# Performance work log

Hardware: AMD Instinct MI355X
Metric: run time of the kernel (lower is better)

The kernel has to match this reference:

```python
import jax, jax.numpy as jnp
import numpy as np

B, I, H, MS, M = 8192, 1024, 1024, 64, 16
TAU = 1.0


def setup_inputs() -> dict:
    key = jax.random.key(0)
    ks = jax.random.split(key, 24)
    s = 0.02
    eps = 1e-6
    return {
        "x": jax.random.normal(ks[0], (B, I), jnp.float32),
        "h": jax.random.normal(ks[1], (B, H), jnp.float32),
        "c": jax.random.normal(ks[2], (B, H), jnp.float32),
        "memory": jax.random.normal(ks[3], (B, M, MS), jnp.float32),
        "u_gs": jax.random.uniform(ks[4], (B, M), jnp.float32, eps, 1.0 - eps),
        "u_a": jax.random.uniform(ks[5], (B, 1), jnp.float32, eps, 1.0 - eps),
        "u_b": jax.random.uniform(ks[6], (B, 1), jnp.float32, eps, 1.0 - eps),
        # pre-concatenated gate weights, matching torch.cat((W_x2*, W_h2*, W_c2*), 0)
        "W_i": jax.random.normal(ks[7], (I + 2 * H, H), jnp.float32) * s,
        "b_i": jnp.zeros((H,), jnp.float32),
        "W_f": jax.random.normal(ks[8], (I + 2 * H, H), jnp.float32) * s,
        "b_f": jnp.ones((H,), jnp.float32),
        "W_o": jax.random.normal(ks[9], (I + 2 * H, H), jnp.float32) * s,
        "b_o": jnp.zeros((H,), jnp.float32),
        "W_cand": jax.random.normal(ks[10], (I + H, H), jnp.float32) * s,
        "b_cand": jnp.zeros((H,), jnp.float32),
        "W_m": jax.random.normal(ks[11], (H, MS), jnp.float32) * s,
        "b_m": jnp.zeros((MS,), jnp.float32),
        "w_a_h": jax.random.normal(ks[12], (H, 1), jnp.float32) * s,
        "w_a_x": jax.random.normal(ks[13], (I, 1), jnp.float32) * s,
        "w_a_r": jax.random.normal(ks[14], (MS, 1), jnp.float32) * s,
        "w_b_h": jax.random.normal(ks[15], (H, 1), jnp.float32) * s,
        "w_b_x": jax.random.normal(ks[16], (I, 1), jnp.float32) * s,
        "w_b_r": jax.random.normal(ks[17], (MS, 1), jnp.float32) * s,
    }


def reference(x, h, c, memory, u_gs, u_a, u_b,
              W_i, b_i, W_f, b_f, W_o, b_o, W_cand, b_cand,
              W_m, b_m, w_a_h, w_a_x, w_a_r, w_b_h, w_b_x, w_b_r):
    # LSTM-style gates with peephole c in the concatenated input
    xhc = jnp.concatenate([x, h, c], axis=1)            # [B, I+2H]
    i = jax.nn.sigmoid(xhc @ W_i + b_i)
    f = jax.nn.sigmoid(xhc @ W_f + b_f)
    cp = jnp.tanh(jnp.concatenate([x, h], axis=1) @ W_cand + b_cand)
    c_new = f * c + i * cp
    o = jax.nn.sigmoid(jnp.concatenate([x, h, c_new], axis=1) @ W_o + b_o)
    h_new = o * jnp.tanh(c_new)

    # memory-slot attention with Gumbel-softmax sampling
    micro = h_new @ W_m + b_m                           # [B, MS]
    logits = jnp.einsum('bmk,bk->bm', memory, micro)    # [B, M]
    g = -jnp.log(-jnp.log(u_gs))                        # Gumbel(0,1)
    attn = jax.nn.softmax((logits + g) / TAU, axis=-1)  # sampled_locations
    sampled = jnp.einsum('bmk,bm->bk', memory, attn) + 1.0  # [B, MS]

    # gumbel-sigmoid (binary concrete) for alpha / beta
    la = jnp.log(u_a) - jnp.log1p(-u_a)
    lb = jnp.log(u_b) - jnp.log1p(-u_b)
    alpha = jax.nn.sigmoid((h_new @ w_a_h + x @ w_a_x + sampled @ w_a_r + la) / TAU)
    beta = jax.nn.sigmoid((h_new @ w_b_h + x @ w_b_x + sampled @ w_b_r + lb) / TAU)

    # [B, 2H+2]
    return jnp.concatenate([h_new, c_new, alpha, beta], axis=1)
```

## Files before the change

### kernel.cpp

```cpp
#include <hip/hip_runtime.h>

typedef __bf16 bfrag __attribute__((ext_vector_type(8)));
typedef float f32x4 __attribute__((ext_vector_type(4)));

#define GLDS16(g, l) __builtin_amdgcn_global_load_lds( \
    (__attribute__((address_space(1))) void*)(g),      \
    (__attribute__((address_space(3))) void*)(l), 16, 0, 0)

__device__ __forceinline__ float bf2f(ushort u) {
    return __uint_as_float(((unsigned)u) << 16);
}
__device__ __forceinline__ ushort f2bf(float f) {
    unsigned u = __float_as_uint(f);
    u += 0x7fff + ((u >> 16) & 1);
    return (ushort)(u >> 16);
}
__device__ __forceinline__ float sigmoidf_(float v) {
    return 1.0f / (1.0f + expf(-v));
}

struct TD { const float* src; ushort* dst; int src_ld; int dst_ld; int ktiles; int off; };
struct TA { TD d[6]; };

__global__ __launch_bounds__(256) void k_prep(const float* __restrict__ x,
                                              const float* __restrict__ h,
                                              const float* __restrict__ c,
                                              ushort* __restrict__ xhcb, TA a,
                                              const float* __restrict__ bi,
                                              const float* __restrict__ bf_,
                                              const float* __restrict__ bc,
                                              const float* __restrict__ bo,
                                              float* __restrict__ Biasf) {
    __shared__ float tile[64][65];
    int bid = blockIdx.x;
    int t = threadIdx.x;
    if (bid < 12288) {
        int idx = bid * 256 + t;
        int row = idx / 384;
        int c8 = (idx - row * 384) * 8;
        const float* s = (c8 < 1024) ? &x[(size_t)row * 1024 + c8]
                       : (c8 < 2048) ? &h[(size_t)row * 1024 + (c8 - 1024)]
                                     : &c[(size_t)row * 1024 + (c8 - 2048)];
        float4 va = *(const float4*)s;
        float4 vb = *(const float4*)(s + 4);
        ushort tmp[8] = {f2bf(va.x), f2bf(va.y), f2bf(va.z), f2bf(va.w),
                         f2bf(vb.x), f2bf(vb.y), f2bf(vb.z), f2bf(vb.w)};
        *(uint4*)&xhcb[(size_t)idx * 8] = *(uint4*)tmp;
    } else if (bid < 15120) {
        int tb = bid - 12288;
        int ri = 0;
#pragma unroll
        for (int i = 1; i < 6; ++i) ri = (tb >= a.d[i].off) ? i : ri;
        const float* src = a.d[ri].src;
        ushort* dst = a.d[ri].dst;
        int src_ld = a.d[ri].src_ld, dst_ld = a.d[ri].dst_ld;
        int local = tb - a.d[ri].off;
        int bx = local % a.d[ri].ktiles;
        int by = local / a.d[ri].ktiles;
        int k0 = bx * 64, n0 = by * 64;
        int c4 = (t & 15) * 4;
        int r = t >> 4;
#pragma unroll
        for (int i = 0; i < 4; ++i) {
            int rr = r + i * 16;
            float4 v = *(const float4*)&src[(size_t)(k0 + rr) * src_ld + n0 + c4];
            tile[rr][c4 + 0] = v.x; tile[rr][c4 + 1] = v.y;
            tile[rr][c4 + 2] = v.z; tile[rr][c4 + 3] = v.w;
        }
        __syncthreads();
        int kk8 = (t & 7) * 8;
        int nn = t >> 3;
#pragma unroll
        for (int i = 0; i < 2; ++i) {
            int n = nn + i * 32;
            ushort tmp[8];
#pragma unroll
            for (int j = 0; j < 8; ++j) tmp[j] = f2bf(tile[kk8 + j][n]);
            *(uint4*)&dst[(size_t)(n0 + n) * dst_ld + k0 + kk8] = *(uint4*)tmp;
        }
    } else {
        int idx = (bid - 15120) * 256 + t;
        int g = idx >> 10, n = idx & 1023;
        const float* s = (g == 0) ? bi : (g == 1) ? bf_ : (g == 2) ? bc : bo;
        Biasf[idx] = s[n];
    }
}

__global__ __launch_bounds__(512) void k_gemm1(const ushort* __restrict__ xhcb,
                                               const ushort* __restrict__ WT,
                                               const float* __restrict__ bias,
                                               ushort* __restrict__ Pre) {
    __shared__ __align__(16) ushort lds[2][32768];
    const int t = threadIdx.x;
    const int m0 = blockIdx.x * 256;
    const int by = blockIdx.y;
    const int n0 = by * 256;
    const int KTOT = (by < 8) ? 3072 : 2048;
    const int NT = KTOT >> 6;
    const int w = t >> 6, l = t & 63;
    const int wr = w >> 2, wc = w & 3;
    const int lane16 = l & 15, quad = l >> 4;
    const int r7 = lane16 & 7;
    const int rowt = t >> 3;
    const int kg = (t & 7) ^ (rowt & 7);
    const int brow_hi = rowt >> 5, brow_lo = rowt & 31;
    f32x4 acc[8][4] = {};
    bfrag afr[4][2];
    bfrag bfr[2][2][2];

    const ushort* Ag = xhcb + (size_t)(m0 + rowt) * 3072 + kg * 8;
    const ushort* Bg = WT + (size_t)(n0 + brow_lo) * 3072 + kg * 8;

#define STAGE_A(BUF, PI, KT)                                                       \
    do {                                                                           \
        GLDS16(Ag + (size_t)((PI) * 64) * 3072 + (KT) * 64,                        \
               &lds[BUF][((PI) * 64) * 64] + t * 8);                               \
        GLDS16(Ag + (size_t)((PI) * 64 + 128) * 3072 + (KT) * 64,                  \
               &lds[BUF][((PI) * 64 + 128) * 64] + t * 8);                         \
    } while (0)

#define STAGE_B(BUF, PI, KT)                                                       \
    do {                                                                           \
        GLDS16(Bg + (size_t)((PI) * 32 + brow_hi * 64) * 3072 + (KT) * 64,         \
               &lds[BUF][16384 + ((PI) * 128) * 64] + t * 8);                      \
        GLDS16(Bg + (size_t)((PI) * 32 + (2 + brow_hi) * 64) * 3072 + (KT) * 64,   \
               &lds[BUF][16384 + ((PI) * 128 + 64) * 64] + t * 8);                 \
    } while (0)

#define LDA(QM)                                                                           \
    do {                                                                                  \
        _Pragma("unroll") for (int ii = 0; ii < 4; ++ii) {                                \
            _Pragma("unroll") for (int h = 0; h < 2; ++h)                                 \
                afr[ii][h] = *(const bfrag*)&Acur[(wr * 128 + (QM) * 64 + ii * 16 + lane16) * 64 + \
                                                  (((h * 4 + quad) ^ r7) * 8)];           \
        }                                                                                 \
    } while (0)

#define LDB(QN)                                                                           \
    do {                                                                                  \
        _Pragma("unroll") for (int jj = 0; jj < 2; ++jj) {                                \
            _Pragma("unroll") for (int h = 0; h < 2; ++h)                                 \
                bfr[QN][jj][h] = *(const bfrag*)&Bcur[((QN) * 128 + wc * 32 + jj * 16 + lane16) * 64 + \
                                                      (((h * 4 + quad) ^ r7) * 8)];       \
        }                                                                                 \
    } while (0)

#define MM(QM, QN)                                                                        \
    do {                                                                                  \
        __builtin_amdgcn_s_setprio(1);                                                    \
        _Pragma("unroll") for (int ii = 0; ii < 4; ++ii) {                                \
            _Pragma("unroll") for (int jj = 0; jj < 2; ++jj) {                            \
                _Pragma("unroll") for (int h = 0; h < 2; ++h)                             \
                    acc[(QM) * 4 + ii][(QN) * 2 + jj] =                                   \
                        __builtin_amdgcn_mfma_f32_16x16x32_bf16(                          \
                            afr[ii][h], bfr[QN][jj][h], acc[(QM) * 4 + ii][(QN) * 2 + jj],\
                            0, 0, 0);                                                     \
            }                                                                             \
        }                                                                                 \
        __builtin_amdgcn_s_setprio(0);                                                    \
    } while (0)

#define BAR_WAIT()                                              \
    do {                                                        \
        __builtin_amdgcn_s_barrier();                           \
        asm volatile("s_waitcnt lgkmcnt(0)" ::: "memory");      \
    } while (0)

    STAGE_A(0, 0, 0); STAGE_B(0, 0, 0);
    STAGE_A(0, 1, 0); STAGE_B(0, 1, 0);
    STAGE_A(1, 0, 1); STAGE_B(1, 0, 1);
    asm volatile("s_waitcnt vmcnt(4)" ::: "memory");
    __builtin_amdgcn_s_barrier();

    for (int kt = 0; kt < NT; ++kt) {
        const int cur = kt & 1;
        const int nxt = cur ^ 1;
        const ushort* Acur = &lds[cur][0];
        const ushort* Bcur = Acur + 16384;
        LDA(0); LDB(0);
        if (kt + 1 < NT) STAGE_A(nxt, 1, kt + 1);
        BAR_WAIT();
        MM(0, 0);
        __builtin_amdgcn_s_barrier();
        LDB(1);
        if (kt + 1 < NT) STAGE_B(nxt, 1, kt + 1);
        BAR_WAIT();
        MM(0, 1);
        __builtin_amdgcn_s_barrier();
        LDA(1);
        if (kt + 2 < NT) STAGE_A(cur, 0, kt + 2);
        BAR_WAIT();
        MM(1, 0);
        __builtin_amdgcn_s_barrier();
        if (kt + 2 < NT) STAGE_B(cur, 0, kt + 2);
        BAR_WAIT();
        MM(1, 1);
        if (kt + 2 < NT) {
            asm volatile("s_waitcnt vmcnt(4)" ::: "memory");
        } else if (kt + 1 < NT) {
            asm volatile("s_waitcnt vmcnt(0)" ::: "memory");
        }
        __builtin_amdgcn_s_barrier();
    }
#undef BAR_WAIT
#undef MM
#undef LDB
#undef LDA
#undef STAGE_B
#undef STAGE_A

#pragma unroll
    for (int i = 0; i < 8; ++i) {
#pragma unroll
        for (int jj = 0; jj < 4; ++jj) {
            int col = n0 + wc * 64 + (jj >> 1) * 32 + (jj & 1) * 16 + lane16;
            float bv = bias[col];
            int rbase = m0 + wr * 128 + i * 16 + quad * 4;
#pragma unroll
            for (int r = 0; r < 4; ++r)
                Pre[(size_t)(rbase + r) * 4096 + col] = f2bf(acc[i][jj][r] + bv);
        }
    }
}

__global__ __launch_bounds__(256) void k_cnew(const ushort* __restrict__ Pre,
                                              const float* __restrict__ cin,
                                              ushort* __restrict__ Cnewb,
                                              float* __restrict__ out) {
    int idx8 = blockIdx.x * 256 + threadIdx.x;
    int b = idx8 >> 7;
    int n8 = (idx8 & 127) * 8;
    uint4 vi = *(const uint4*)(Pre + (size_t)b * 4096 + n8);
    uint4 vf = *(const uint4*)(Pre + (size_t)b * 4096 + 1024 + n8);
    uint4 vc = *(const uint4*)(Pre + (size_t)b * 4096 + 2048 + n8);
    float4 c0 = *(const float4*)(cin + (size_t)b * 1024 + n8);
    float4 c1 = *(const float4*)(cin + (size_t)b * 1024 + n8 + 4);
    const ushort* pi = (const ushort*)&vi;
    const ushort* pf = (const ushort*)&vf;
    const ushort* pc = (const ushort*)&vc;
    float cv[8] = {c0.x, c0.y, c0.z, c0.w, c1.x, c1.y, c1.z, c1.w};
    float cn[8];
    ushort cb[8];
#pragma unroll
    for (int j = 0; j < 8; ++j) {
        float iv = sigmoidf_(bf2f(pi[j]));
        float fv = sigmoidf_(bf2f(pf[j]));
        float cp = tanhf(bf2f(pc[j]));
        cn[j] = fv * cv[j] + iv * cp;
        cb[j] = f2bf(cn[j]);
    }
    *(uint4*)(Cnewb + (size_t)b * 1024 + n8) = *(uint4*)cb;
    float* orow = out + (size_t)b * 2050 + 1024 + n8;
#pragma unroll
    for (int j = 0; j < 4; ++j)
        *(float2*)(orow + j * 2) = make_float2(cn[j * 2], cn[j * 2 + 1]);
}

__global__ __launch_bounds__(256) void k_gemm2(const ushort* __restrict__ Cnewb,
                                               const ushort* __restrict__ WoCT,
                                               const ushort* __restrict__ Pre,
                                               ushort* __restrict__ Hnewb,
                                               float* __restrict__ out) {
    __shared__ __align__(16) ushort As[128 * 64];
    __shared__ __align__(16) ushort Bs[128 * 64];
    int t = threadIdx.x;
    int m0 = blockIdx.x * 128, n0 = blockIdx.y * 128;
    int w = t >> 6, l = t & 63;
    int wm = (w & 1) * 64, wn = (w >> 1) * 64;
    int lane16 = l & 15, quad = l >> 4;
    int rowt = t >> 3;
    int kg = (t & 7) ^ (rowt & 7);
    int r7 = lane16 & 7;
    f32x4 acc[4][4] = {};

    const ushort* Abase = Cnewb + (size_t)(m0 + rowt) * 1024 + kg * 8;
    const ushort* Bbase = WoCT + (size_t)(n0 + rowt) * 1024 + kg * 8;

    for (int k0 = 0; k0 < 1024; k0 += 64) {
#pragma unroll
        for (int q = 0; q < 4; ++q)
            GLDS16(Abase + (size_t)q * 32 * 1024 + k0, As + q * 2048 + t * 8);
#pragma unroll
        for (int q = 0; q < 4; ++q)
            GLDS16(Bbase + (size_t)q * 32 * 1024 + k0, Bs + q * 2048 + t * 8);
        __syncthreads();
#pragma unroll
        for (int hh = 0; hh < 2; ++hh) {
            int slot8 = ((hh * 4 + quad) ^ r7) * 8;
            bfrag af[4], bfr[4];
#pragma unroll
            for (int i = 0; i < 4; ++i) {
                af[i]  = *(const bfrag*)&As[(wm + i * 16 + lane16) * 64 + slot8];
                bfr[i] = *(const bfrag*)&Bs[(wn + i * 16 + lane16) * 64 + slot8];
            }
#pragma unroll
            for (int i = 0; i < 4; ++i)
#pragma unroll
                for (int j = 0; j < 4; ++j)
                    acc[i][j] = __builtin_amdgcn_mfma_f32_16x16x32_bf16(af[i], bfr[j], acc[i][j], 0, 0, 0);
        }
        __syncthreads();
    }
#pragma unroll
    for (int i = 0; i < 4; ++i) {
#pragma unroll
        for (int j = 0; j < 4; ++j) {
            int col = n0 + wn + j * 16 + lane16;
            int rbase = m0 + wm + i * 16 + quad * 4;
#pragma unroll
            for (int r = 0; r < 4; ++r) {
                int row = rbase + r;
                float opre = acc[i][j][r] + bf2f(Pre[(size_t)row * 4096 + 3072 + col]);
                float o = sigmoidf_(opre);
                float cnv = bf2f(Cnewb[(size_t)row * 1024 + col]);
                float hv = o * tanhf(cnv);
                Hnewb[(size_t)row * 1024 + col] = f2bf(hv);
                out[(size_t)row * 2050 + col] = hv;
            }
        }
    }
}

__global__ __launch_bounds__(256) void k_attn(
    const ushort* __restrict__ Hnewb, const float* __restrict__ outr,
    const float* __restrict__ x, const float* __restrict__ memory,
    const float* __restrict__ u_gs, const float* __restrict__ u_a,
    const float* __restrict__ u_b, const ushort* __restrict__ WmT,
    const float* __restrict__ b_m,
    const float* __restrict__ w_a_h, const float* __restrict__ w_a_x,
    const float* __restrict__ w_a_r, const float* __restrict__ w_b_h,
    const float* __restrict__ w_b_x, const float* __restrict__ w_b_r,
    float* __restrict__ out) {
    __shared__ float sMicro[16 * 64];
    __shared__ float sAttn[16 * 16];
    __shared__ float sSamp[16 * 64];

    int b0 = blockIdx.x * 16;
    int t = threadIdx.x;
    int w = t >> 6, l = t & 63;
    int lane16 = l & 15, quad = l >> 4;

    {
        f32x4 acc = {0.f, 0.f, 0.f, 0.f};
        const ushort* Ab = Hnewb + (size_t)(b0 + lane16) * 1024 + quad * 8;
        const ushort* Bb = WmT + (size_t)(w * 16 + lane16) * 1024 + quad * 8;
#pragma unroll 4
        for (int k0 = 0; k0 < 1024; k0 += 32) {
            bfrag av = *(const bfrag*)(Ab + k0);
            bfrag bv = *(const bfrag*)(Bb + k0);
            acc = __builtin_amdgcn_mfma_f32_16x16x32_bf16(av, bv, acc, 0, 0, 0);
        }
        float bm = b_m[w * 16 + lane16];
#pragma unroll
        for (int r = 0; r < 4; ++r)
            sMicro[(quad * 4 + r) * 64 + w * 16 + lane16] = acc[r] + bm;
    }
    __syncthreads();

    {
        int r = t >> 4, m = t & 15;
        const float4* mem4 = (const float4*)(memory + (size_t)(b0 + r) * 1024 + m * 64);
        float lg = 0.f;
#pragma unroll
        for (int k4 = 0; k4 < 16; ++k4) {
            float4 mv = mem4[k4];
            const float* sm = &sMicro[r * 64 + k4 * 4];
            lg += mv.x * sm[0] + mv.y * sm[1] + mv.z * sm[2] + mv.w * sm[3];
        }
        float u = u_gs[(b0 + r) * 16 + m];
        float z = lg - logf(-logf(u));
        float zm = z;
        for (int off = 8; off; off >>= 1) zm = fmaxf(zm, __shfl_xor(zm, off, 16));
        float p = expf(z - zm);
        float ps = p;
        for (int off = 8; off; off >>= 1) ps += __shfl_xor(ps, off, 16);
        sAttn[r * 16 + m] = p / ps;
    }
    __syncthreads();

#pragma unroll
    for (int q = 0; q < 4; ++q) {
        int r = w * 4 + q;
        const float* mem = memory + (size_t)(b0 + r) * 1024 + l;
        float s = 0.f;
#pragma unroll
        for (int m = 0; m < 16; ++m) s += sAttn[r * 16 + m] * mem[m * 64];
        sSamp[r * 64 + l] = s + 1.0f;
    }
    __syncthreads();

    {
        int r = t >> 4, s16 = t & 15;
        size_t hoff = (size_t)(b0 + r) * 2050;
        size_t xoff = (size_t)(b0 + r) * 1024;
        float za = 0.f, zb = 0.f;
        for (int kk = 0; kk < 64; ++kk) {
            int k = s16 + kk * 16;
            float hv = outr[hoff + k];
            float xv = x[xoff + k];
            za += hv * w_a_h[k] + xv * w_a_x[k];
            zb += hv * w_b_h[k] + xv * w_b_x[k];
        }
#pragma unroll
        for (int k = s16 * 4; k < s16 * 4 + 4; ++k) {
            float sv = sSamp[r * 64 + k];
            za += sv * w_a_r[k];
            zb += sv * w_b_r[k];
        }
        for (int off = 8; off; off >>= 1) {
            za += __shfl_xor(za, off, 16);
            zb += __shfl_xor(zb, off, 16);
        }
        if (s16 == 0) {
            float ua = u_a[b0 + r];
            float ub = u_b[b0 + r];
            float la = logf(ua) - log1pf(-ua);
            float lb = logf(ub) - log1pf(-ub);
            out[(size_t)(b0 + r) * 2050 + 2048] = sigmoidf_(za + la);
            out[(size_t)(b0 + r) * 2050 + 2049] = sigmoidf_(zb + lb);
        }
    }
}

extern "C" void kernel_launch(void* const* d_in, const int* in_sizes, int n_in,
                              void* d_out, int out_size, void* d_ws, size_t ws_size,
                              hipStream_t stream) {
    const float* x      = (const float*)d_in[0];
    const float* h      = (const float*)d_in[1];
    const float* c      = (const float*)d_in[2];
    const float* memory = (const float*)d_in[3];
    const float* u_gs   = (const float*)d_in[4];
    const float* u_a    = (const float*)d_in[5];
    const float* u_b    = (const float*)d_in[6];
    const float* W_i    = (const float*)d_in[7];
    const float* b_i    = (const float*)d_in[8];
    const float* W_f    = (const float*)d_in[9];
    const float* b_f    = (const float*)d_in[10];
    const float* W_o    = (const float*)d_in[11];
    const float* b_o    = (const float*)d_in[12];
    const float* W_cand = (const float*)d_in[13];
    const float* b_cand = (const float*)d_in[14];
    const float* W_m    = (const float*)d_in[15];
    const float* b_m    = (const float*)d_in[16];
    const float* w_a_h  = (const float*)d_in[17];
    const float* w_a_x  = (const float*)d_in[18];
    const float* w_a_r  = (const float*)d_in[19];
    const float* w_b_h  = (const float*)d_in[20];
    const float* w_b_x  = (const float*)d_in[21];
    const float* w_b_r  = (const float*)d_in[22];
    float* out = (float*)d_out;

    char* ws = (char*)d_ws;
    ushort* WT    = (ushort*)(ws);
    ushort* WoCT  = (ushort*)(ws + 25165824);
    ushort* Pre   = (ushort*)(ws + 27262976);
    ushort* xhcb  = (ushort*)(ws + 94371840);
    float*  Biasf = (float*)(ws + 144703488);
    ushort* WmT   = (ushort*)(ws + 144719872);
    ushort* Cnewb = xhcb;
    ushort* Hnewb = WT;

    TA ta;
    ta.d[0] = {W_i,                       WT,                        1024, 3072, 48, 0};
    ta.d[1] = {W_f,                       WT + (size_t)1024 * 3072,  1024, 3072, 48, 768};
    ta.d[2] = {W_cand,                    WT + (size_t)2048 * 3072,  1024, 3072, 32, 1536};
    ta.d[3] = {W_o,                       WT + (size_t)3072 * 3072,  1024, 3072, 32, 2048};
    ta.d[4] = {W_o + (size_t)2048 * 1024, WoCT,                      1024, 1024, 16, 2560};
    ta.d[5] = {W_m,                       WmT,                         64, 1024, 16, 2816};

    k_prep<<<15136, 256, 0, stream>>>(x, h, c, xhcb, ta, b_i, b_f, b_cand, b_o, Biasf);

    k_gemm1<<<dim3(32, 16), 512, 0, stream>>>(xhcb, WT, Biasf, Pre);
    k_cnew<<<4096, 256, 0, stream>>>(Pre, c, Cnewb, out);
    k_gemm2<<<dim3(64, 8), 256, 0, stream>>>(Cnewb, WoCT, Pre, Hnewb, out);
    k_attn<<<512, 256, 0, stream>>>(Hnewb, out, x, memory, u_gs, u_a, u_b, WmT, b_m,
                                    w_a_h, w_a_x, w_a_r, w_b_h, w_b_x, w_b_r, out);
}
```

Before: 479.6 us.

## Split gate GEMM MFMA phases by K-half and drop explicit LDS waits

```diff
diff --git a/kernel.cpp b/kernel.cpp
--- a/kernel.cpp
+++ b/kernel.cpp
@@ -105,8 +105,6 @@
     const int kg = (t & 7) ^ (rowt & 7);
     const int brow_hi = rowt >> 5, brow_lo = rowt & 31;
     f32x4 acc[8][4] = {};
-    bfrag afr[4][2];
-    bfrag bfr[2][2][2];
 
     const ushort* Ag = xhcb + (size_t)(m0 + rowt) * 3072 + kg * 8;
     const ushort* Bg = WT + (size_t)(n0 + brow_lo) * 3072 + kg * 8;
@@ -127,43 +125,29 @@
                &lds[BUF][16384 + ((PI) * 128 + 64) * 64] + t * 8);                 \
     } while (0)
 
-#define LDA(QM)                                                                           \
+#define LDAF(dst, QM, H)                                                                  \
     do {                                                                                  \
-        _Pragma("unroll") for (int ii = 0; ii < 4; ++ii) {                                \
-            _Pragma("unroll") for (int h = 0; h < 2; ++h)                                 \
-                afr[ii][h] = *(const bfrag*)&Acur[(wr * 128 + (QM) * 64 + ii * 16 + lane16) * 64 + \
-                                                  (((h * 4 + quad) ^ r7) * 8)];           \
-        }                                                                                 \
+        _Pragma("unroll") for (int ii = 0; ii < 4; ++ii)                                  \
+            dst[ii] = *(const bfrag*)&Acur[(wr * 128 + (QM) * 64 + ii * 16 + lane16) * 64 + \
+                                           ((((H) * 4 + quad) ^ r7) * 8)];                \
     } while (0)
 
-#define LDB(QN)                                                                           \
+#define LDBF(dst, H)                                                                      \
     do {                                                                                  \
-        _Pragma("unroll") for (int jj = 0; jj < 2; ++jj) {                                \
-            _Pragma("unroll") for (int h = 0; h < 2; ++h)                                 \
-                bfr[QN][jj][h] = *(const bfrag*)&Bcur[((QN) * 128 + wc * 32 + jj * 16 + lane16) * 64 + \
-                                                      (((h * 4 + quad) ^ r7) * 8)];       \
-        }                                                                                 \
+        _Pragma("unroll") for (int jj = 0; jj < 4; ++jj)                                  \
+            dst[jj] = *(const bfrag*)&Bcur[((jj >> 1) * 128 + wc * 32 + (jj & 1) * 16 + lane16) * 64 + \
+                                           ((((H) * 4 + quad) ^ r7) * 8)];                \
     } while (0)
 
-#define MM(QM, QN)                                                                        \
+#define MMH(QM, AH, BH)                                                                   \
     do {                                                                                  \
         __builtin_amdgcn_s_setprio(1);                                                    \
         _Pragma("unroll") for (int ii = 0; ii < 4; ++ii) {                                \
-            _Pragma("unroll") for (int jj = 0; jj < 2; ++jj) {                            \
-                _Pragma("unroll") for (int h = 0; h < 2; ++h)                             \
-                    acc[(QM) * 4 + ii][(QN) * 2 + jj] =                                   \
-                        __builtin_amdgcn_mfma_f32_16x16x32_bf16(                          \
-                            afr[ii][h], bfr[QN][jj][h], acc[(QM) * 4 + ii][(QN) * 2 + jj],\
-                            0, 0, 0);                                                     \
-            }                                                                             \
+            _Pragma("unroll") for (int jj = 0; jj < 4; ++jj)                              \
+                acc[(QM) * 4 + ii][jj] = __builtin_amdgcn_mfma_f32_16x16x32_bf16(         \
+                    AH[ii], BH[jj], acc[(QM) * 4 + ii][jj], 0, 0, 0);                     \
         }                                                                                 \
         __builtin_amdgcn_s_setprio(0);                                                    \
-    } while (0)
-
-#define BAR_WAIT()                                              \
-    do {                                                        \
-        __builtin_amdgcn_s_barrier();                           \
-        asm volatile("s_waitcnt lgkmcnt(0)" ::: "memory");      \
     } while (0)
 
     STAGE_A(0, 0, 0); STAGE_B(0, 0, 0);
@@ -177,24 +161,22 @@
         const int nxt = cur ^ 1;
         const ushort* Acur = &lds[cur][0];
         const ushort* Bcur = Acur + 16384;
-        LDA(0); LDB(0);
+        bfrag a0h0[4], a0h1[4], a1h0[4], a1h1[4], bh0[4], bh1[4];
+        LDAF(a0h0, 0, 0); LDBF(bh0, 0);
+        LDAF(a0h1, 0, 1); LDBF(bh1, 1);
         if (kt + 1 < NT) STAGE_A(nxt, 1, kt + 1);
-        BAR_WAIT();
-        MM(0, 0);
+        MMH(0, a0h0, bh0);
         __builtin_amdgcn_s_barrier();
-        LDB(1);
+        LDAF(a1h0, 1, 0);
         if (kt + 1 < NT) STAGE_B(nxt, 1, kt + 1);
-        BAR_WAIT();
-        MM(0, 1);
+        MMH(0, a0h1, bh1);
         __builtin_amdgcn_s_barrier();
-        LDA(1);
+        LDAF(a1h1, 1, 1);
         if (kt + 2 < NT) STAGE_A(cur, 0, kt + 2);
-        BAR_WAIT();
-        MM(1, 0);
+        MMH(1, a1h0, bh0);
         __builtin_amdgcn_s_barrier();
         if (kt + 2 < NT) STAGE_B(cur, 0, kt + 2);
-        BAR_WAIT();
-        MM(1, 1);
+        MMH(1, a1h1, bh1);
         if (kt + 2 < NT) {
             asm volatile("s_waitcnt vmcnt(4)" ::: "memory");
         } else if (kt + 1 < NT) {
@@ -202,10 +184,9 @@
         }
         __builtin_amdgcn_s_barrier();
     }
-#undef BAR_WAIT
-#undef MM
-#undef LDB
-#undef LDA
+#undef MMH
+#undef LDBF
+#undef LDAF
 #undef STAGE_B
 #undef STAGE_A
 
```

Result: no change. 476.2 us (-0.7%).
